# Kernel tuning notes

Measured on AMD Instinct MI355X. Metric: run time of the kernel, lower is better.

## Reference

```python
import jax, jax.numpy as jnp
import numpy as np

THETA = 0.7  # init kwarg theta

def setup_inputs() -> dict:
    key = jax.random.key(0)
    k1, k2, k3 = jax.random.split(key, 3)
    B, Cin, Cout, H, Wd = 32, 128, 128, 128, 128
    x = jax.random.normal(k1, (B, Cin, H, Wd), dtype=jnp.float32)
    W = jax.random.normal(k2, (Cout, Cin, 3, 3), dtype=jnp.float32) * (2.0 / (Cin * 9)) ** 0.5
    b = jax.random.normal(k3, (Cout,), dtype=jnp.float32) * 0.01
    return {"x": x, "W": W, "b": b}

def reference(x, W, b):
    # main conv: 3x3, stride 1, zero padding 1 (NCHW / OIHW)
    norm_out = jax.lax.conv_general_dilated(
        x, W, window_strides=(1, 1), padding=((1, 1), (1, 1)),
        dimension_numbers=("NCHW", "OIHW", "NCHW"))
    norm_out = norm_out + b[None, :, None, None]
    # central-difference stencil ('ca' cross mask [[0,1,0],[1,-4,1],[0,1,0]]),
    # identical for all (out,in) channel pairs -> apply once to channel sum.
    s = jnp.sum(x, axis=1, keepdims=True)  # [B,1,H,W]
    p = jnp.pad(s, ((0, 0), (0, 0), (1, 1), (1, 1)), mode="edge")  # replicate pad
    diff = (p[:, :, :-2, 1:-1] + p[:, :, 2:, 1:-1]
            + p[:, :, 1:-1, :-2] + p[:, :, 1:-1, 2:] - 4.0 * s)  # [B,1,H,W]
    # diff broadcasts over out_channels (mask repeated across channels)
    return norm_out - THETA * diff
```

## Files before the change

### kernel.cpp

```cpp
#include <hip/hip_runtime.h>
#include <hip/hip_bf16.h>


typedef __attribute__((ext_vector_type(8))) int int8v;
typedef __attribute__((ext_vector_type(16))) float f32x16;

#define THETA 0.7f
#define XT_OFF   0
#define WP_OFF   134217728ull
#define S_OFF    (134217728ull + 294912ull)

__device__ __forceinline__ unsigned f2e4m3(float x) {
  unsigned u = __builtin_bit_cast(unsigned, x);
  unsigned s = (u >> 24) & 0x80u;
  unsigned au = u & 0x7FFFFFFFu;
  if (au >= 0x43E80000u) return s | 0x7Eu;
  if (au < 0x3C800000u) {
    float q = __builtin_bit_cast(float, au) * 512.0f;
    return s | (unsigned)(int)(q + 0.5f);
  }
  unsigned m = au + 0x000FFFFFu + ((au >> 20) & 1u);
  int e = (int)(m >> 23) - 127;
  unsigned mant = (m >> 20) & 7u;
  if (e > 8 || (e == 8 && mant == 7u)) return s | 0x7Eu;
  return s | ((unsigned)(e + 7) << 3) | mant;
}

__device__ __forceinline__ void gload_lds16(const void* g, void* l) {
  __builtin_amdgcn_global_load_lds(
      (const __attribute__((address_space(1))) unsigned int*)g,
      (__attribute__((address_space(3))) unsigned int*)l, 16, 0, 0);
}

__global__ void pack_w_kernel(const float* __restrict__ w, char* __restrict__ wp) {
  const int co = blockIdx.x, ci = threadIdx.x;
  const float* src = w + ((size_t)co * 128 + ci) * 9;
  const int kp = ci >> 5, r = ci & 31;
  const int half = (r >> 4) & 1, kb = (r >> 3) & 1, j = r & 7;
  #pragma unroll
  for (int tap = 0; tap < 9; ++tap) {
    const unsigned char bv = (unsigned char)f2e4m3(src[tap] * 16.0f);
    wp[(size_t)((tap * 4 + kp) * 2 + kb) * 2048 + co * 16 + half * 8 + j] = bv;
  }
}

__global__ __launch_bounds__(256)
void transpose_sum_kernel(const float* __restrict__ x, char* __restrict__ xt,
                          float* __restrict__ s) {
  __shared__ float tile[64][129];
  __shared__ float s2[2][128];
  const int h = blockIdx.x, b = blockIdx.y;
  const int t = threadIdx.x;
  s2[t >> 7][t & 127] = 0.f;
  char* rowb = xt + (size_t)(b * 128 + h) * 16384;

  #pragma unroll
  for (int p = 0; p < 2; ++p) {
    __syncthreads();
    {
      const int ciq = t >> 5;
      const int wq = (t & 31) << 2;
      #pragma unroll
      for (int i = 0; i < 8; ++i) {
        const int cil = i * 8 + ciq;
        const int ci = p * 64 + cil;
        const float4 v = *(const float4*)(x + (((size_t)(b * 128 + ci) * 128 + h) * 128 + wq));
        tile[cil][wq] = v.x; tile[cil][wq + 1] = v.y;
        tile[cil][wq + 2] = v.z; tile[cil][wq + 3] = v.w;
      }
    }
    __syncthreads();
    {
      const int w = t & 127, hseg = t >> 7;
      float a = 0.f;
      #pragma unroll 8
      for (int j = 0; j < 32; ++j) a += tile[hseg * 32 + j][w];
      s2[hseg][w] += a;
    }
    #pragma unroll
    for (int i = 0; i < 2; ++i) {
      const int u = i * 256 + t;
      const int lc = u >> 7;
      const int w = u & 127;
      const int base = (lc >> 1) * 32 + (lc & 1) * 8;
      unsigned wd[4];
      #pragma unroll
      for (int half = 0; half < 2; ++half) {
        const int c0 = base + half * 16;
        int lo = __builtin_amdgcn_cvt_pk_fp8_f32(tile[c0 + 0][w], tile[c0 + 1][w], 0, false);
        lo = __builtin_amdgcn_cvt_pk_fp8_f32(tile[c0 + 2][w], tile[c0 + 3][w], lo, true);
        int hi = __builtin_amdgcn_cvt_pk_fp8_f32(tile[c0 + 4][w], tile[c0 + 5][w], 0, false);
        hi = __builtin_amdgcn_cvt_pk_fp8_f32(tile[c0 + 6][w], tile[c0 + 7][w], hi, true);
        wd[half * 2] = (unsigned)lo; wd[half * 2 + 1] = (unsigned)hi;
      }
      *(uint4*)(rowb + (size_t)(p * 512 + u) * 16) = make_uint4(wd[0], wd[1], wd[2], wd[3]);
    }
  }
  __syncthreads();
  if (t < 128) s[(size_t)(b * 128 + h) * 128 + t] = s2[0][t] + s2[1][t];
}

__global__ __launch_bounds__(256, 3)
void conv_mfma_kernel(const char* __restrict__ xt, const char* __restrict__ wp,
                      const float* __restrict__ bias, const float* __restrict__ s,
                      float* __restrict__ out) {
  __shared__ uint4 xs4[3 * 8 * 130];
  char* xs = (char*)xs4;

  const int bid = blockIdx.x;
  const int sw = (bid & 7) * 512 + (bid >> 3);
  const int h = sw & 127;
  const int b = sw >> 7;

  const int t = threadIdx.x;
  const int lane = t & 63, wave = t >> 6;
  const int wm = wave >> 1, wn = wave & 1;
  const int l31 = lane & 31, kb = lane >> 5;

  f32x16 acc[2][2];
  #pragma unroll
  for (int mt = 0; mt < 2; ++mt)
    #pragma unroll
    for (int nt = 0; nt < 2; ++nt)
      #pragma unroll
      for (int r = 0; r < 16; ++r)
        acc[mt][nt][r] = 0.f;

  if (t < 48) {
    const int row = t >> 4, k = t & 15, chunk = k >> 1, side = k & 1;
    xs4[row * 1040 + chunk * 130 + side * 129] = make_uint4(0u, 0u, 0u, 0u);
  }
  #pragma unroll
  for (int r = 0; r < 3; ++r) {
    const int hh = h - 1 + r;
    if ((unsigned)hh < 128u) {
      const char* rb = xt + (size_t)(b * 128 + hh) * 16384;
      #pragma unroll
      for (int i = 0; i < 4; ++i) {
        const int u = i * 256 + t;
        const int chunk = u >> 7, w = u & 127;
        gload_lds16(rb + (size_t)u * 16,
                    xs + (size_t)(r * 1040 + chunk * 130 + 1 + w) * 16);
      }
    } else {
      #pragma unroll
      for (int i = 0; i < 5; ++i) {
        const int u = i * 256 + t;
        if (u < 1040) xs4[r * 1040 + u] = make_uint4(0u, 0u, 0u, 0u);
      }
    }
  }
  __syncthreads();

  #pragma unroll
  for (int kh = 0; kh < 3; ++kh) {
    const char* xrow = xs + kh * 16640;
    #pragma unroll
    for (int dxi = 0; dxi < 3; ++dxi) {
      const int tap = kh * 3 + dxi;
      const char* wb = wp + (size_t)(tap * 8) * 2048;
      #pragma unroll
      for (int kp2 = 0; kp2 < 2; ++kp2) {
        const int c0 = (kp2 * 2 + kb) * 2;
        int8v av[2];
        #pragma unroll
        for (int mt = 0; mt < 2; ++mt) {
          const uint4 lo = *(const uint4*)(wb + (size_t)c0 * 2048 +
                                           (wm * 64 + mt * 32 + l31) * 16);
          const uint4 hi = *(const uint4*)(wb + (size_t)(c0 + 1) * 2048 +
                                           (wm * 64 + mt * 32 + l31) * 16);
          av[mt] = (int8v){(int)lo.x, (int)lo.y, (int)lo.z, (int)lo.w,
                           (int)hi.x, (int)hi.y, (int)hi.z, (int)hi.w};
        }
        int8v bv[2];
        #pragma unroll
        for (int nt = 0; nt < 2; ++nt) {
          const int g = wn * 64 + nt * 32 + l31 + dxi;
          const uint4 lo = *(const uint4*)(xrow + (size_t)(c0 * 130 + g) * 16);
          const uint4 hi = *(const uint4*)(xrow + (size_t)((c0 + 1) * 130 + g) * 16);
          bv[nt] = (int8v){(int)lo.x, (int)lo.y, (int)lo.z, (int)lo.w,
                           (int)hi.x, (int)hi.y, (int)hi.z, (int)hi.w};
        }
        #pragma unroll
        for (int mt = 0; mt < 2; ++mt)
          #pragma unroll
          for (int nt = 0; nt < 2; ++nt)
            acc[mt][nt] = __builtin_amdgcn_mfma_scale_f32_32x32x64_f8f6f4(
                av[mt], bv[nt], acc[mt][nt],
                0 , 0 ,
                0, 0x7F7F7F7Fu ,
                0, 0x7F7F7F7Fu );
      }
    }
  }

  const float* sb = s + (size_t)b * 16384;
  float dif[2];
  #pragma unroll
  for (int nt = 0; nt < 2; ++nt) {
    const int w = wn * 64 + nt * 32 + l31;
    const float sc = sb[h * 128 + w];
    const float up = sb[(h > 0 ? h - 1 : 0) * 128 + w];
    const float dn = sb[(h < 127 ? h + 1 : 127) * 128 + w];
    const float lf = sb[h * 128 + (w > 0 ? w - 1 : 0)];
    const float rt = sb[h * 128 + (w < 127 ? w + 1 : 127)];
    dif[nt] = up + dn + lf + rt - 4.0f * sc;
  }
  #pragma unroll
  for (int mt = 0; mt < 2; ++mt) {
    #pragma unroll
    for (int r = 0; r < 16; ++r) {
      const int co = wm * 64 + mt * 32 + (r & 3) + 8 * (r >> 2) + 4 * kb;
      const float bv = bias[co];
      float* orow = out + ((size_t)(b * 128 + co) * 128 + h) * 128;
      #pragma unroll
      for (int nt = 0; nt < 2; ++nt) {
        const int w = wn * 64 + nt * 32 + l31;
        orow[w] = acc[mt][nt][r] * 0.0625f + bv - THETA * dif[nt];
      }
    }
  }
}

extern "C" void kernel_launch(void* const* d_in, const int* in_sizes, int n_in,
                              void* d_out, int out_size, void* d_ws, size_t ws_size,
                              hipStream_t stream) {
  const float* x = (const float*)d_in[0];
  const float* W = (const float*)d_in[1];
  const float* bias = (const float*)d_in[2];
  float* out = (float*)d_out;
  char* ws = (char*)d_ws;
  char* xt = ws + XT_OFF;
  char* wp = ws + WP_OFF;
  float* s = (float*)(ws + S_OFF);
  pack_w_kernel<<<dim3(128), dim3(128), 0, stream>>>(W, wp);
  transpose_sum_kernel<<<dim3(128, 32), dim3(256), 0, stream>>>(x, xt, s);
  conv_mfma_kernel<<<dim3(4096), dim3(256), 0, stream>>>(xt, wp, bias, s, out);
}
```

Baseline: 187.4 us.

## Split conv input staging into two channel halves to halve LDS and raise occupancy

The conv kernel now stages the three input rows in two passes of 64 channels each, reusing a half-size LDS buffer, and raises the launch-bounds occupancy hint from 3 to 4 blocks per CU. The aim is to fit more resident blocks per CU so memory latency is better hidden. In exchange each block adds two extra barriers and serializes the second load behind the first compute with no overlap, and the higher occupancy target tightens the register budget.

```diff
diff --git a/kernel.cpp b/kernel.cpp
--- a/kernel.cpp
+++ b/kernel.cpp
@@ -100,11 +100,11 @@
   if (t < 128) s[(size_t)(b * 128 + h) * 128 + t] = s2[0][t] + s2[1][t];
 }
 
-__global__ __launch_bounds__(256, 3)
+__global__ __launch_bounds__(256, 4)
 void conv_mfma_kernel(const char* __restrict__ xt, const char* __restrict__ wp,
                       const float* __restrict__ bias, const float* __restrict__ s,
                       float* __restrict__ out) {
-  __shared__ uint4 xs4[3 * 8 * 130];
+  __shared__ uint4 xs4[3 * 4 * 130];
   char* xs = (char*)xs4;
 
   const int bid = blockIdx.x;
@@ -126,49 +126,48 @@
       for (int r = 0; r < 16; ++r)
         acc[mt][nt][r] = 0.f;
 
-  if (t < 48) {
-    const int row = t >> 4, k = t & 15, chunk = k >> 1, side = k & 1;
-    xs4[row * 1040 + chunk * 130 + side * 129] = make_uint4(0u, 0u, 0u, 0u);
-  }
-  #pragma unroll
-  for (int r = 0; r < 3; ++r) {
-    const int hh = h - 1 + r;
-    if ((unsigned)hh < 128u) {
-      const char* rb = xt + (size_t)(b * 128 + hh) * 16384;
-      #pragma unroll
-      for (int i = 0; i < 4; ++i) {
-        const int u = i * 256 + t;
-        const int chunk = u >> 7, w = u & 127;
-        gload_lds16(rb + (size_t)u * 16,
-                    xs + (size_t)(r * 1040 + chunk * 130 + 1 + w) * 16);
-      }
-    } else {
-      #pragma unroll
-      for (int i = 0; i < 5; ++i) {
-        const int u = i * 256 + t;
-        if (u < 1040) xs4[r * 1040 + u] = make_uint4(0u, 0u, 0u, 0u);
-      }
-    }
-  }
-  __syncthreads();
-
-  #pragma unroll
-  for (int kh = 0; kh < 3; ++kh) {
-    const char* xrow = xs + kh * 16640;
-    #pragma unroll
-    for (int dxi = 0; dxi < 3; ++dxi) {
-      const int tap = kh * 3 + dxi;
-      const char* wb = wp + (size_t)(tap * 8) * 2048;
-      #pragma unroll
-      for (int kp2 = 0; kp2 < 2; ++kp2) {
-        const int c0 = (kp2 * 2 + kb) * 2;
+  if (t < 24) {
+    const int row = t >> 3, k = t & 7, chunk = k >> 1, side = k & 1;
+    xs4[(row * 4 + chunk) * 130 + side * 129] = make_uint4(0u, 0u, 0u, 0u);
+  }
+
+  auto stage_half = [&](int kp2) {
+    #pragma unroll
+    for (int r = 0; r < 3; ++r) {
+      const int hh = h - 1 + r;
+      if ((unsigned)hh < 128u) {
+        const char* rb = xt + (size_t)(b * 128 + hh) * 16384 + (size_t)kp2 * 8192;
+        #pragma unroll
+        for (int i = 0; i < 2; ++i) {
+          const int u = i * 256 + t;
+          const int chunk = u >> 7, w = u & 127;
+          gload_lds16(rb + (size_t)u * 16,
+                      xs + (size_t)((r * 4 + chunk) * 130 + 1 + w) * 16);
+        }
+      } else {
+        #pragma unroll
+        for (int i = 0; i < 2; ++i) {
+          const int u = i * 256 + t;
+          const int chunk = u >> 7, w = u & 127;
+          xs4[(r * 4 + chunk) * 130 + 1 + w] = make_uint4(0u, 0u, 0u, 0u);
+        }
+      }
+    }
+  };
+
+  auto compute_half = [&](int kp2) {
+    #pragma unroll
+    for (int kh = 0; kh < 3; ++kh) {
+      const char* xrow = xs + kh * 8320;
+      #pragma unroll
+      for (int dxi = 0; dxi < 3; ++dxi) {
+        const int tap = kh * 3 + dxi;
+        const char* wb = wp + (size_t)(tap * 8 + kp2 * 4 + kb * 2) * 2048;
         int8v av[2];
         #pragma unroll
         for (int mt = 0; mt < 2; ++mt) {
-          const uint4 lo = *(const uint4*)(wb + (size_t)c0 * 2048 +
-                                           (wm * 64 + mt * 32 + l31) * 16);
-          const uint4 hi = *(const uint4*)(wb + (size_t)(c0 + 1) * 2048 +
-                                           (wm * 64 + mt * 32 + l31) * 16);
+          const uint4 lo = *(const uint4*)(wb + (wm * 64 + mt * 32 + l31) * 16);
+          const uint4 hi = *(const uint4*)(wb + 2048 + (wm * 64 + mt * 32 + l31) * 16);
           av[mt] = (int8v){(int)lo.x, (int)lo.y, (int)lo.z, (int)lo.w,
                            (int)hi.x, (int)hi.y, (int)hi.z, (int)hi.w};
         }
@@ -176,8 +175,8 @@
         #pragma unroll
         for (int nt = 0; nt < 2; ++nt) {
           const int g = wn * 64 + nt * 32 + l31 + dxi;
-          const uint4 lo = *(const uint4*)(xrow + (size_t)(c0 * 130 + g) * 16);
-          const uint4 hi = *(const uint4*)(xrow + (size_t)((c0 + 1) * 130 + g) * 16);
+          const uint4 lo = *(const uint4*)(xrow + (size_t)(kb * 2 * 130 + g) * 16);
+          const uint4 hi = *(const uint4*)(xrow + (size_t)((kb * 2 + 1) * 130 + g) * 16);
           bv[nt] = (int8v){(int)lo.x, (int)lo.y, (int)lo.z, (int)lo.w,
                            (int)hi.x, (int)hi.y, (int)hi.z, (int)hi.w};
         }
@@ -192,7 +191,15 @@
                 0, 0x7F7F7F7Fu );
       }
     }
-  }
+  };
+
+  stage_half(0);
+  __syncthreads();
+  compute_half(0);
+  __syncthreads();
+  stage_half(1);
+  __syncthreads();
+  compute_half(1);
 
   const float* sb = s + (size_t)b * 16384;
   float dif[2];
```

Result: slower. 299.6 us (+59.8%).

## Split conv output row into two 64-wide halves per block

Applied to the files above, without the earlier changes.

Each conv block now computes half an output row (64 columns) instead of a full row. This halves LDS usage and accumulator registers so launch bounds can request 4 blocks per SM, and it doubles the grid to 8192 blocks. Halo columns come from neighbouring global data with a direct load instead of zero fill. In exchange, weight fragments are reused across only one N-tile per wave, so global and L2 weight reads per MFMA double, and there are more, smaller output stores.

```diff
diff --git a/kernel.cpp b/kernel.cpp
--- a/kernel.cpp
+++ b/kernel.cpp
@@ -100,124 +100,110 @@
   if (t < 128) s[(size_t)(b * 128 + h) * 128 + t] = s2[0][t] + s2[1][t];
 }
 
-__global__ __launch_bounds__(256, 3)
+__global__ __launch_bounds__(256, 4)
 void conv_mfma_kernel(const char* __restrict__ xt, const char* __restrict__ wp,
                       const float* __restrict__ bias, const float* __restrict__ s,
                       float* __restrict__ out) {
-  __shared__ uint4 xs4[3 * 8 * 130];
+  __shared__ uint4 xs4[3 * 8 * 66];
   char* xs = (char*)xs4;
 
   const int bid = blockIdx.x;
-  const int sw = (bid & 7) * 512 + (bid >> 3);
-  const int h = sw & 127;
-  const int b = sw >> 7;
+  const int sw = (bid & 7) * 1024 + (bid >> 3);
+  const int whalf = sw & 1;
+  const int h = (sw >> 1) & 127;
+  const int b = sw >> 8;
 
   const int t = threadIdx.x;
   const int lane = t & 63, wave = t >> 6;
   const int wm = wave >> 1, wn = wave & 1;
   const int l31 = lane & 31, kb = lane >> 5;
 
-  f32x16 acc[2][2];
+  f32x16 acc[2];
   #pragma unroll
   for (int mt = 0; mt < 2; ++mt)
     #pragma unroll
-    for (int nt = 0; nt < 2; ++nt)
-      #pragma unroll
-      for (int r = 0; r < 16; ++r)
-        acc[mt][nt][r] = 0.f;
+    for (int r = 0; r < 16; ++r)
+      acc[mt][r] = 0.f;
+
+  const char* xrow_g = xt + (size_t)(b * 128) * 16384;
 
   if (t < 48) {
-    const int row = t >> 4, k = t & 15, chunk = k >> 1, side = k & 1;
-    xs4[row * 1040 + chunk * 130 + side * 129] = make_uint4(0u, 0u, 0u, 0u);
-  }
-  #pragma unroll
-  for (int r = 0; r < 3; ++r) {
+    const int row = t >> 4, k = t & 15, c = k >> 1, side = k & 1;
+    const int hh = h - 1 + row;
+    const int gw = whalf * 64 - 1 + side * 65;
+    uint4 v = make_uint4(0u, 0u, 0u, 0u);
+    if ((unsigned)hh < 128u && (unsigned)gw < 128u)
+      v = *(const uint4*)(xrow_g + (size_t)hh * 16384 + ((size_t)c * 128 + gw) * 16);
+    xs4[(row * 8 + c) * 66 + side * 65] = v;
+  }
+  #pragma unroll
+  for (int i = 0; i < 6; ++i) {
+    const int u = i * 256 + t;
+    const int r = u >> 9, rem = u & 511;
+    const int c = rem >> 6, wl = rem & 63;
     const int hh = h - 1 + r;
+    char* dst = xs + (size_t)((r * 8 + c) * 66 + 1 + wl) * 16;
     if ((unsigned)hh < 128u) {
-      const char* rb = xt + (size_t)(b * 128 + hh) * 16384;
-      #pragma unroll
-      for (int i = 0; i < 4; ++i) {
-        const int u = i * 256 + t;
-        const int chunk = u >> 7, w = u & 127;
-        gload_lds16(rb + (size_t)u * 16,
-                    xs + (size_t)(r * 1040 + chunk * 130 + 1 + w) * 16);
-      }
+      gload_lds16(xrow_g + (size_t)hh * 16384 +
+                  ((size_t)c * 128 + whalf * 64 + wl) * 16, dst);
     } else {
-      #pragma unroll
-      for (int i = 0; i < 5; ++i) {
-        const int u = i * 256 + t;
-        if (u < 1040) xs4[r * 1040 + u] = make_uint4(0u, 0u, 0u, 0u);
-      }
+      *(uint4*)dst = make_uint4(0u, 0u, 0u, 0u);
     }
   }
   __syncthreads();
 
   #pragma unroll
   for (int kh = 0; kh < 3; ++kh) {
-    const char* xrow = xs + kh * 16640;
+    const char* xrow = xs + kh * 8 * 66 * 16;
     #pragma unroll
     for (int dxi = 0; dxi < 3; ++dxi) {
       const int tap = kh * 3 + dxi;
-      const char* wb = wp + (size_t)(tap * 8) * 2048;
       #pragma unroll
       for (int kp2 = 0; kp2 < 2; ++kp2) {
-        const int c0 = (kp2 * 2 + kb) * 2;
+        const int c0 = kp2 * 4 + kb * 2;
+        const char* wb = wp + (size_t)(tap * 8 + c0) * 2048;
         int8v av[2];
         #pragma unroll
         for (int mt = 0; mt < 2; ++mt) {
-          const uint4 lo = *(const uint4*)(wb + (size_t)c0 * 2048 +
-                                           (wm * 64 + mt * 32 + l31) * 16);
-          const uint4 hi = *(const uint4*)(wb + (size_t)(c0 + 1) * 2048 +
-                                           (wm * 64 + mt * 32 + l31) * 16);
+          const uint4 lo = *(const uint4*)(wb + (wm * 64 + mt * 32 + l31) * 16);
+          const uint4 hi = *(const uint4*)(wb + 2048 + (wm * 64 + mt * 32 + l31) * 16);
           av[mt] = (int8v){(int)lo.x, (int)lo.y, (int)lo.z, (int)lo.w,
                            (int)hi.x, (int)hi.y, (int)hi.z, (int)hi.w};
         }
-        int8v bv[2];
-        #pragma unroll
-        for (int nt = 0; nt < 2; ++nt) {
-          const int g = wn * 64 + nt * 32 + l31 + dxi;
-          const uint4 lo = *(const uint4*)(xrow + (size_t)(c0 * 130 + g) * 16);
-          const uint4 hi = *(const uint4*)(xrow + (size_t)((c0 + 1) * 130 + g) * 16);
-          bv[nt] = (int8v){(int)lo.x, (int)lo.y, (int)lo.z, (int)lo.w,
-                           (int)hi.x, (int)hi.y, (int)hi.z, (int)hi.w};
-        }
+        const int gi = wn * 32 + l31 + dxi;
+        const uint4 lo = *(const uint4*)(xrow + (size_t)(c0 * 66 + gi) * 16);
+        const uint4 hi = *(const uint4*)(xrow + (size_t)((c0 + 1) * 66 + gi) * 16);
+        const int8v bv = (int8v){(int)lo.x, (int)lo.y, (int)lo.z, (int)lo.w,
+                                 (int)hi.x, (int)hi.y, (int)hi.z, (int)hi.w};
         #pragma unroll
         for (int mt = 0; mt < 2; ++mt)
-          #pragma unroll
-          for (int nt = 0; nt < 2; ++nt)
-            acc[mt][nt] = __builtin_amdgcn_mfma_scale_f32_32x32x64_f8f6f4(
-                av[mt], bv[nt], acc[mt][nt],
-                0 , 0 ,
-                0, 0x7F7F7F7Fu ,
-                0, 0x7F7F7F7Fu );
+          acc[mt] = __builtin_amdgcn_mfma_scale_f32_32x32x64_f8f6f4(
+              av[mt], bv, acc[mt],
+              0 , 0 ,
+              0, 0x7F7F7F7Fu ,
+              0, 0x7F7F7F7Fu );
       }
     }
   }
 
   const float* sb = s + (size_t)b * 16384;
-  float dif[2];
-  #pragma unroll
-  for (int nt = 0; nt < 2; ++nt) {
-    const int w = wn * 64 + nt * 32 + l31;
+  const int w = whalf * 64 + wn * 32 + l31;
+  float dif;
+  {
     const float sc = sb[h * 128 + w];
     const float up = sb[(h > 0 ? h - 1 : 0) * 128 + w];
     const float dn = sb[(h < 127 ? h + 1 : 127) * 128 + w];
     const float lf = sb[h * 128 + (w > 0 ? w - 1 : 0)];
     const float rt = sb[h * 128 + (w < 127 ? w + 1 : 127)];
-    dif[nt] = up + dn + lf + rt - 4.0f * sc;
+    dif = up + dn + lf + rt - 4.0f * sc;
   }
   #pragma unroll
   for (int mt = 0; mt < 2; ++mt) {
     #pragma unroll
     for (int r = 0; r < 16; ++r) {
       const int co = wm * 64 + mt * 32 + (r & 3) + 8 * (r >> 2) + 4 * kb;
-      const float bv = bias[co];
-      float* orow = out + ((size_t)(b * 128 + co) * 128 + h) * 128;
-      #pragma unroll
-      for (int nt = 0; nt < 2; ++nt) {
-        const int w = wn * 64 + nt * 32 + l31;
-        orow[w] = acc[mt][nt][r] * 0.0625f + bv - THETA * dif[nt];
-      }
+      out[((size_t)(b * 128 + co) * 128 + h) * 128 + w] =
+          acc[mt][r] * 0.0625f + bias[co] - THETA * dif;
     }
   }
 }
@@ -235,5 +221,5 @@
   float* s = (float*)(ws + S_OFF);
   pack_w_kernel<<<dim3(128), dim3(128), 0, stream>>>(W, wp);
   transpose_sum_kernel<<<dim3(128, 32), dim3(256), 0, stream>>>(x, xt, s);
-  conv_mfma_kernel<<<dim3(4096), dim3(256), 0, stream>>>(xt, wp, bias, s, out);
-}
+  conv_mfma_kernel<<<dim3(8192), dim3(256), 0, stream>>>(xt, wp, bias, s, out);
+}
```

Measured after the change: 309.5 us. +65.1%, slower.

## Fuse fp8 transpose and channel-sum into conv kernel, drop intermediate buffers

Applied to the files above, without the earlier changes.

Removes the separate transpose/sum kernel. The conv kernel now loads fp32 input rows straight into LDS, converts them to fp8 in its own layout, and accumulates the channel sums for the stencil. The K dimension is split into two halves so the smaller LDS buffer is reused. This avoids writing and re-reading the fp8 copy and the sum array in global memory. The cost is that each input row is loaded and converted by three blocks, and loading, conversion and MFMA are now serialized behind many barriers with no overlap.

```diff
diff --git a/kernel.cpp b/kernel.cpp
--- a/kernel.cpp
+++ b/kernel.cpp
@@ -6,9 +6,6 @@
 typedef __attribute__((ext_vector_type(16))) float f32x16;
 
 #define THETA 0.7f
-#define XT_OFF   0
-#define WP_OFF   134217728ull
-#define S_OFF    (134217728ull + 294912ull)
 
 __device__ __forceinline__ unsigned f2e4m3(float x) {
   unsigned u = __builtin_bit_cast(unsigned, x);
@@ -44,67 +41,12 @@
   }
 }
 
-__global__ __launch_bounds__(256)
-void transpose_sum_kernel(const float* __restrict__ x, char* __restrict__ xt,
-                          float* __restrict__ s) {
-  __shared__ float tile[64][129];
-  __shared__ float s2[2][128];
-  const int h = blockIdx.x, b = blockIdx.y;
-  const int t = threadIdx.x;
-  s2[t >> 7][t & 127] = 0.f;
-  char* rowb = xt + (size_t)(b * 128 + h) * 16384;
-
-  #pragma unroll
-  for (int p = 0; p < 2; ++p) {
-    __syncthreads();
-    {
-      const int ciq = t >> 5;
-      const int wq = (t & 31) << 2;
-      #pragma unroll
-      for (int i = 0; i < 8; ++i) {
-        const int cil = i * 8 + ciq;
-        const int ci = p * 64 + cil;
-        const float4 v = *(const float4*)(x + (((size_t)(b * 128 + ci) * 128 + h) * 128 + wq));
-        tile[cil][wq] = v.x; tile[cil][wq + 1] = v.y;
-        tile[cil][wq + 2] = v.z; tile[cil][wq + 3] = v.w;
-      }
-    }
-    __syncthreads();
-    {
-      const int w = t & 127, hseg = t >> 7;
-      float a = 0.f;
-      #pragma unroll 8
-      for (int j = 0; j < 32; ++j) a += tile[hseg * 32 + j][w];
-      s2[hseg][w] += a;
-    }
-    #pragma unroll
-    for (int i = 0; i < 2; ++i) {
-      const int u = i * 256 + t;
-      const int lc = u >> 7;
-      const int w = u & 127;
-      const int base = (lc >> 1) * 32 + (lc & 1) * 8;
-      unsigned wd[4];
-      #pragma unroll
-      for (int half = 0; half < 2; ++half) {
-        const int c0 = base + half * 16;
-        int lo = __builtin_amdgcn_cvt_pk_fp8_f32(tile[c0 + 0][w], tile[c0 + 1][w], 0, false);
-        lo = __builtin_amdgcn_cvt_pk_fp8_f32(tile[c0 + 2][w], tile[c0 + 3][w], lo, true);
-        int hi = __builtin_amdgcn_cvt_pk_fp8_f32(tile[c0 + 4][w], tile[c0 + 5][w], 0, false);
-        hi = __builtin_amdgcn_cvt_pk_fp8_f32(tile[c0 + 6][w], tile[c0 + 7][w], hi, true);
-        wd[half * 2] = (unsigned)lo; wd[half * 2 + 1] = (unsigned)hi;
-      }
-      *(uint4*)(rowb + (size_t)(p * 512 + u) * 16) = make_uint4(wd[0], wd[1], wd[2], wd[3]);
-    }
-  }
-  __syncthreads();
-  if (t < 128) s[(size_t)(b * 128 + h) * 128 + t] = s2[0][t] + s2[1][t];
-}
-
 __global__ __launch_bounds__(256, 3)
-void conv_mfma_kernel(const char* __restrict__ xt, const char* __restrict__ wp,
-                      const float* __restrict__ bias, const float* __restrict__ s,
-                      float* __restrict__ out) {
-  __shared__ uint4 xs4[3 * 8 * 130];
+void conv_mfma_kernel(const float* __restrict__ x, const char* __restrict__ wp,
+                      const float* __restrict__ bias, float* __restrict__ out) {
+  __shared__ uint4 xs4[3 * 4 * 130];
+  __shared__ float tile[32][128];
+  __shared__ float srow[3][128];
   char* xs = (char*)xs4;
 
   const int bid = blockIdx.x;
@@ -126,58 +68,83 @@
       for (int r = 0; r < 16; ++r)
         acc[mt][nt][r] = 0.f;
 
-  if (t < 48) {
-    const int row = t >> 4, k = t & 15, chunk = k >> 1, side = k & 1;
-    xs4[row * 1040 + chunk * 130 + side * 129] = make_uint4(0u, 0u, 0u, 0u);
-  }
-  #pragma unroll
-  for (int r = 0; r < 3; ++r) {
-    const int hh = h - 1 + r;
-    if ((unsigned)hh < 128u) {
-      const char* rb = xt + (size_t)(b * 128 + hh) * 16384;
-      #pragma unroll
-      for (int i = 0; i < 4; ++i) {
-        const int u = i * 256 + t;
-        const int chunk = u >> 7, w = u & 127;
-        gload_lds16(rb + (size_t)u * 16,
-                    xs + (size_t)(r * 1040 + chunk * 130 + 1 + w) * 16);
-      }
-    } else {
-      #pragma unroll
-      for (int i = 0; i < 5; ++i) {
-        const int u = i * 256 + t;
-        if (u < 1040) xs4[r * 1040 + u] = make_uint4(0u, 0u, 0u, 0u);
+  if (t < 24) {
+    const int row = t >> 3, k = t & 7, c = k >> 1, side = k & 1;
+    xs4[(row * 4 + c) * 130 + side * 129] = make_uint4(0u, 0u, 0u, 0u);
+  }
+  if (t < 128) { srow[0][t] = 0.f; srow[1][t] = 0.f; srow[2][t] = 0.f; }
+
+  const char* xb = (const char*)x;
+
+  #pragma unroll
+  for (int kp2 = 0; kp2 < 2; ++kp2) {
+    #pragma unroll
+    for (int r = 0; r < 3; ++r) {
+      const int hh = h - 1 + r;
+      const bool inb = (unsigned)hh < 128u;
+      #pragma unroll
+      for (int kpl = 0; kpl < 2; ++kpl) {
+        const int kp = kp2 * 2 + kpl;
+        __syncthreads();
+        if (inb) {
+          #pragma unroll
+          for (int i = 0; i < 4; ++i) {
+            const int u = i * 256 + t;
+            const int ci = u >> 5, wq = (u & 31) << 2;
+            gload_lds16(xb + ((((size_t)(b * 128 + kp * 32 + ci) * 128 + hh) * 128 + wq) * 4),
+                        (char*)tile + (size_t)u * 16);
+          }
+        }
+        __syncthreads();
+        const int c_l = t >> 7, w = t & 127;
+        unsigned wd[4];
+        if (inb) {
+          #pragma unroll
+          for (int half = 0; half < 2; ++half) {
+            const int b0 = half * 16 + c_l * 8;
+            int lo = __builtin_amdgcn_cvt_pk_fp8_f32(tile[b0 + 0][w], tile[b0 + 1][w], 0, false);
+            lo = __builtin_amdgcn_cvt_pk_fp8_f32(tile[b0 + 2][w], tile[b0 + 3][w], lo, true);
+            int hi = __builtin_amdgcn_cvt_pk_fp8_f32(tile[b0 + 4][w], tile[b0 + 5][w], 0, false);
+            hi = __builtin_amdgcn_cvt_pk_fp8_f32(tile[b0 + 6][w], tile[b0 + 7][w], hi, true);
+            wd[half * 2] = (unsigned)lo; wd[half * 2 + 1] = (unsigned)hi;
+          }
+          if (t < 128) {
+            float a = 0.f;
+            #pragma unroll 8
+            for (int j = 0; j < 32; ++j) a += tile[j][t];
+            srow[r][t] += a;
+          }
+        } else {
+          wd[0] = wd[1] = wd[2] = wd[3] = 0u;
+        }
+        xs4[(r * 4 + kpl * 2 + c_l) * 130 + 1 + w] =
+            make_uint4(wd[0], wd[1], wd[2], wd[3]);
       }
     }
-  }
-  __syncthreads();
-
-  #pragma unroll
-  for (int kh = 0; kh < 3; ++kh) {
-    const char* xrow = xs + kh * 16640;
-    #pragma unroll
-    for (int dxi = 0; dxi < 3; ++dxi) {
-      const int tap = kh * 3 + dxi;
-      const char* wb = wp + (size_t)(tap * 8) * 2048;
-      #pragma unroll
-      for (int kp2 = 0; kp2 < 2; ++kp2) {
-        const int c0 = (kp2 * 2 + kb) * 2;
+    __syncthreads();
+
+    #pragma unroll
+    for (int kh = 0; kh < 3; ++kh) {
+      const char* xrow = xs + (size_t)kh * 4 * 130 * 16;
+      #pragma unroll
+      for (int dxi = 0; dxi < 3; ++dxi) {
+        const int tap = kh * 3 + dxi;
+        const char* wb = wp + (size_t)(tap * 8 + kp2 * 4 + kb * 2) * 2048;
         int8v av[2];
         #pragma unroll
         for (int mt = 0; mt < 2; ++mt) {
-          const uint4 lo = *(const uint4*)(wb + (size_t)c0 * 2048 +
-                                           (wm * 64 + mt * 32 + l31) * 16);
-          const uint4 hi = *(const uint4*)(wb + (size_t)(c0 + 1) * 2048 +
-                                           (wm * 64 + mt * 32 + l31) * 16);
+          const uint4 lo = *(const uint4*)(wb + (wm * 64 + mt * 32 + l31) * 16);
+          const uint4 hi = *(const uint4*)(wb + 2048 + (wm * 64 + mt * 32 + l31) * 16);
           av[mt] = (int8v){(int)lo.x, (int)lo.y, (int)lo.z, (int)lo.w,
                            (int)hi.x, (int)hi.y, (int)hi.z, (int)hi.w};
         }
+        const int c0 = kb * 2;
         int8v bv[2];
         #pragma unroll
         for (int nt = 0; nt < 2; ++nt) {
-          const int g = wn * 64 + nt * 32 + l31 + dxi;
-          const uint4 lo = *(const uint4*)(xrow + (size_t)(c0 * 130 + g) * 16);
-          const uint4 hi = *(const uint4*)(xrow + (size_t)((c0 + 1) * 130 + g) * 16);
+          const int gi = wn * 64 + nt * 32 + l31 + dxi;
+          const uint4 lo = *(const uint4*)(xrow + (size_t)(c0 * 130 + gi) * 16);
+          const uint4 hi = *(const uint4*)(xrow + (size_t)((c0 + 1) * 130 + gi) * 16);
           bv[nt] = (int8v){(int)lo.x, (int)lo.y, (int)lo.z, (int)lo.w,
                            (int)hi.x, (int)hi.y, (int)hi.z, (int)hi.w};
         }
@@ -194,29 +161,27 @@
     }
   }
 
-  const float* sb = s + (size_t)b * 16384;
   float dif[2];
   #pragma unroll
   for (int nt = 0; nt < 2; ++nt) {
     const int w = wn * 64 + nt * 32 + l31;
-    const float sc = sb[h * 128 + w];
-    const float up = sb[(h > 0 ? h - 1 : 0) * 128 + w];
-    const float dn = sb[(h < 127 ? h + 1 : 127) * 128 + w];
-    const float lf = sb[h * 128 + (w > 0 ? w - 1 : 0)];
-    const float rt = sb[h * 128 + (w < 127 ? w + 1 : 127)];
-    dif[nt] = up + dn + lf + rt - 4.0f * sc;
+    const float up = srow[h > 0 ? 0 : 1][w];
+    const float dn = srow[h < 127 ? 2 : 1][w];
+    const float lf = srow[1][w > 0 ? w - 1 : 0];
+    const float rt = srow[1][w < 127 ? w + 1 : 127];
+    dif[nt] = up + dn + lf + rt - 4.0f * srow[1][w];
   }
   #pragma unroll
   for (int mt = 0; mt < 2; ++mt) {
     #pragma unroll
     for (int r = 0; r < 16; ++r) {
       const int co = wm * 64 + mt * 32 + (r & 3) + 8 * (r >> 2) + 4 * kb;
-      const float bv = bias[co];
+      const float bvl = bias[co];
       float* orow = out + ((size_t)(b * 128 + co) * 128 + h) * 128;
       #pragma unroll
       for (int nt = 0; nt < 2; ++nt) {
         const int w = wn * 64 + nt * 32 + l31;
-        orow[w] = acc[mt][nt][r] * 0.0625f + bv - THETA * dif[nt];
+        orow[w] = acc[mt][nt][r] * 0.0625f + bvl - THETA * dif[nt];
       }
     }
   }
@@ -229,11 +194,7 @@
   const float* W = (const float*)d_in[1];
   const float* bias = (const float*)d_in[2];
   float* out = (float*)d_out;
-  char* ws = (char*)d_ws;
-  char* xt = ws + XT_OFF;
-  char* wp = ws + WP_OFF;
-  float* s = (float*)(ws + S_OFF);
+  char* wp = (char*)d_ws;
   pack_w_kernel<<<dim3(128), dim3(128), 0, stream>>>(W, wp);
-  transpose_sum_kernel<<<dim3(128, 32), dim3(256), 0, stream>>>(x, xt, s);
-  conv_mfma_kernel<<<dim3(4096), dim3(256), 0, stream>>>(xt, wp, bias, s, out);
-}
+  conv_mfma_kernel<<<dim3(4096), dim3(256), 0, stream>>>(x, wp, bias, out);
+}
```

New measurement: 478.0 us. 155% more time.
